# Kernel tuning notes

Measured on AMD Instinct MI355X. Metric: run time of the kernel, lower is better.

Reference implementation:

```python
import jax, jax.numpy as jnp
import numpy as np

F = 32          # fmap_size = (256 // 16) * 2
WIN = F // 8 - 1  # window = 3
HID = 160
HID4 = 640
N = 4096
Q = 16


def setup_inputs() -> dict:
    key = jax.random.key(0)
    ks = jax.random.split(key, 24)

    def lin(k, i, o):
        return jax.random.normal(k, (i, o), jnp.float32) * (1.0 / np.sqrt(i))

    return {
        "feature_pos": jax.random.normal(ks[0], (N, Q, HID), jnp.float32),
        "query_embedding": jax.random.normal(ks[1], (N, Q, HID), jnp.float32),
        "attn_matrix": jax.random.normal(ks[2], (N, Q, F * F), jnp.float32),
        "ws1": lin(ks[3], HID, HID4), "bs1": jnp.zeros((HID4,), jnp.float32),
        "ws2": lin(ks[4], HID4, HID4), "bs2": jnp.zeros((HID4,), jnp.float32),
        "ws3": lin(ks[5], HID4, HID4), "bs3": jnp.zeros((HID4,), jnp.float32),
        "ws4": lin(ks[6], HID4, 1), "bs4": jnp.zeros((1,), jnp.float32),
        "wp1": lin(ks[7], HID, HID4), "bp1": jnp.zeros((HID4,), jnp.float32),
        "wp2": lin(ks[8], HID4, HID4), "bp2": jnp.zeros((HID4,), jnp.float32),
        "wp3": lin(ks[9], HID4, HID4), "bp3": jnp.zeros((HID4,), jnp.float32),
        "wp4": lin(ks[10], HID4, 4), "bp4": jnp.zeros((4,), jnp.float32),
    }


def _mlp(x, w1, b1, w2, b2, w3, b3, w4, b4):
    h = jax.nn.relu(x @ w1 + b1)
    h = jax.nn.relu(h @ w2 + b2)
    h = jax.nn.relu(h @ w3 + b3)
    return h @ w4 + b4


def _gauss_blur3(x):
    # torchvision GaussianBlur(3, sigma=1.0): separable 3-tap, reflect padding
    e = np.exp(-0.5)
    k = jnp.asarray([e, 1.0, e], jnp.float32) / np.float32(1.0 + 2.0 * e)
    xp = jnp.pad(x, ((0, 0), (1, 1), (0, 0)), mode="reflect")
    x = k[0] * xp[:, :-2] + k[1] * xp[:, 1:-1] + k[2] * xp[:, 2:]
    xp = jnp.pad(x, ((0, 0), (0, 0), (1, 1)), mode="reflect")
    return k[0] * xp[:, :, :-2] + k[1] * xp[:, :, 1:-1] + k[2] * xp[:, :, 2:]


def _process_attnmap(am):
    # am: [N, F, F]
    n = am.shape[0]
    ab = _gauss_blur3(am)
    ab = (ab - ab.mean(axis=(1, 2), keepdims=True)) / jnp.std(ab, axis=(1, 2), keepdims=True, ddof=1)
    idx = jnp.argmax(ab.reshape(n, -1), axis=1)
    px = (idx % F).astype(jnp.int32)
    py = (idx // F).astype(jnp.int32)
    # vectorized windowed mean of clamped sigmoid (masked instead of per-sample slicing)
    s = jnp.clip(jax.nn.sigmoid(am), 1e-4, 1.0 - 1e-4)
    pos = jnp.arange(F)
    colmask = ((pos[None, :] >= jnp.maximum(0, px - WIN)[:, None]) &
               (pos[None, :] < jnp.minimum(F, px + WIN)[:, None])).astype(s.dtype)  # [N,F]
    rowmask = ((pos[None, :] >= jnp.maximum(0, py - WIN)[:, None]) &
               (pos[None, :] < jnp.minimum(F, py + WIN)[:, None])).astype(s.dtype)
    colsum = s.sum(axis=1)  # [N,F] sum over rows -> per-column totals
    rowsum = s.sum(axis=2)  # [N,F] sum over cols -> per-row totals
    tempx = (colsum * colmask).sum(axis=1) / (F * colmask.sum(axis=1))
    tempy = (rowsum * rowmask).sum(axis=1) / (F * rowmask.sum(axis=1))
    prepos = jnp.stack([px, py], axis=1).astype(jnp.float32)          # [N,2]
    presize = jnp.stack([tempx, tempy], axis=1) * np.float32(F)        # [N,2]
    return prepos, presize


def reference(feature_pos, query_embedding, attn_matrix,
              ws1, bs1, ws2, bs2, ws3, bs3, ws4, bs4,
              wp1, bp1, wp2, bp2, wp3, bp3, wp4, bp4):
    n = query_embedding.shape[0]
    qe = query_embedding.mean(axis=1)   # [N, HID]
    fp = feature_pos.mean(axis=1)       # [N, HID]
    am = attn_matrix.mean(axis=1).reshape(n, F, F)
    score = _mlp(qe, ws1, bs1, ws2, bs2, ws3, bs3, ws4, bs4).reshape(n)
    bbox_info = _mlp(fp, wp1, bp1, wp2, bp2, wp3, bp3, wp4, bp4)  # [N,4]
    sizeoffset = jnp.clip(bbox_info[:, :2], -2.0, 2.0)
    posoffset = jnp.clip(bbox_info[:, 2:], -2.0, 2.0)
    prepos, presize = _process_attnmap(am)
    xy = (prepos + posoffset) / np.float32(F)
    wh = (presize + sizeoffset) / np.float32(F)
    xy = xy - 0.5 * wh  # predict_center
    bbox = jnp.concatenate([xy, wh], axis=1)
    return bbox, score
```

## Files before the change

### kernel.cpp

```cpp
#include <hip/hip_runtime.h>
#include <hip/hip_bf16.h>
#include <stdint.h>

#define HID 160
#define HID4 640
#define FDIM 32
#define NPIX 1024

#define GK0 0.27406862f
#define GK1 0.45186276f

typedef __attribute__((ext_vector_type(8))) short short8;
typedef __attribute__((ext_vector_type(4))) float f32x4;

__device__ __forceinline__ ushort f2b(float f) {
  union { float f; uint32_t u; } v; v.f = f;
  uint32_t u = v.u;
  u += 0x7fffu + ((u >> 16) & 1u);
  return (ushort)(u >> 16);
}
__device__ __forceinline__ float b2f(ushort s) {
  union { uint32_t u; float f; } v; v.u = ((uint32_t)s) << 16;
  return v.f;
}

__global__ __launch_bounds__(256) void attn_kernel(const float* __restrict__ attn,
                                                   float* __restrict__ pp) {
  const int n = blockIdx.x;
  const int tid = threadIdx.x;
  __shared__ float am[FDIM][FDIM + 1];
  __shared__ float tmp[FDIM][FDIM + 1];
  __shared__ float bl[FDIM][FDIM + 1];
  __shared__ float rowsum[FDIM], colsum[FDIM];
  __shared__ float redv[4];
  __shared__ int redi[4];

  const float* base = attn + (size_t)n * (16 * NPIX);
  float4 a = make_float4(0.f, 0.f, 0.f, 0.f);
#pragma unroll
  for (int q = 0; q < 16; ++q) {
    float4 v = *(const float4*)(base + q * NPIX + tid * 4);
    a.x += v.x; a.y += v.y; a.z += v.z; a.w += v.w;
  }
  {
    const int f0 = tid * 4;
    const int r = f0 >> 5, c = f0 & 31;
    am[r][c + 0] = a.x * 0.0625f;
    am[r][c + 1] = a.y * 0.0625f;
    am[r][c + 2] = a.z * 0.0625f;
    am[r][c + 3] = a.w * 0.0625f;
  }
  __syncthreads();
  for (int f = tid; f < NPIX; f += 256) {
    int r = f >> 5, c = f & 31;
    int rm = (r == 0) ? 1 : r - 1;
    int rp = (r == 31) ? 30 : r + 1;
    tmp[r][c] = GK0 * am[rm][c] + GK1 * am[r][c] + GK0 * am[rp][c];
  }
  __syncthreads();
  for (int f = tid; f < NPIX; f += 256) {
    int r = f >> 5, c = f & 31;
    int cm = (c == 0) ? 1 : c - 1;
    int cp = (c == 31) ? 30 : c + 1;
    bl[r][c] = GK0 * tmp[r][cm] + GK1 * tmp[r][c] + GK0 * tmp[r][cp];
  }
  __syncthreads();
  float bv = -1e30f; int bi = 0;
  for (int f = tid; f < NPIX; f += 256) {
    float v = bl[f >> 5][f & 31];
    if (v > bv || (v == bv && f < bi)) { bv = v; bi = f; }
  }
  for (int off = 32; off > 0; off >>= 1) {
    float ov = __shfl_down(bv, off);
    int oi = __shfl_down(bi, off);
    if (ov > bv || (ov == bv && oi < bi)) { bv = ov; bi = oi; }
  }
  if ((tid & 63) == 0) { redv[tid >> 6] = bv; redi[tid >> 6] = bi; }
  for (int f = tid; f < NPIX; f += 256) {
    int r = f >> 5, c = f & 31;
    float s = 1.f / (1.f + expf(-am[r][c]));
    tmp[r][c] = fminf(fmaxf(s, 1e-4f), 0.9999f);
  }
  __syncthreads();
  if (tid < 32) {
    float s = 0.f;
    for (int c = 0; c < 32; ++c) s += tmp[tid][c];
    rowsum[tid] = s;
  } else if (tid < 64) {
    int c = tid - 32;
    float s = 0.f;
    for (int r = 0; r < 32; ++r) s += tmp[r][c];
    colsum[c] = s;
  }
  __syncthreads();
  if (tid == 0) {
    float bestv = redv[0]; int besti = redi[0];
    for (int w = 1; w < 4; ++w)
      if (redv[w] > bestv || (redv[w] == bestv && redi[w] < besti)) {
        bestv = redv[w]; besti = redi[w];
      }
    int px = besti & 31, py = besti >> 5;
    int c0 = max(0, px - 3), c1 = min(32, px + 3);
    float sx = 0.f;
    for (int c = c0; c < c1; ++c) sx += colsum[c];
    float psx = (sx / (32.f * (float)(c1 - c0))) * 32.f;
    int r0 = max(0, py - 3), r1 = min(32, py + 3);
    float sy = 0.f;
    for (int r = r0; r < r1; ++r) sy += rowsum[r];
    float psy = (sy / (32.f * (float)(r1 - r0))) * 32.f;
    pp[n * 4 + 0] = (float)px;
    pp[n * 4 + 1] = (float)py;
    pp[n * 4 + 2] = psx;
    pp[n * 4 + 3] = psy;
  }
}

__global__ __launch_bounds__(256) void mean_kernel(const float* __restrict__ qemb,
                                                   const float* __restrict__ fpos,
                                                   ushort* __restrict__ qe_b,
                                                   ushort* __restrict__ fp_b,
                                                   int total) {
  int idx = blockIdx.x * 256 + threadIdx.x;
  if (idx >= 2 * total) return;
  const float* src; ushort* dst; int i;
  if (idx < total) { src = qemb; dst = qe_b; i = idx; }
  else             { src = fpos; dst = fp_b; i = idx - total; }
  int nn = i / HID, h = i - nn * HID;
  const float* p = src + (size_t)nn * (16 * HID) + h;
  float s = 0.f;
#pragma unroll
  for (int q = 0; q < 16; ++q) s += p[q * HID];
  dst[i] = f2b(s * 0.0625f);
}

__global__ __launch_bounds__(256) void transpose_cast(const float* __restrict__ in,
                                                      ushort* __restrict__ out, int K) {
  __shared__ float t[32][33];
  const int bx = blockIdx.x * 32;
  const int by = blockIdx.y * 32;
  const int lx = threadIdx.x;
  const int ly = threadIdx.y;
#pragma unroll
  for (int i = 0; i < 4; ++i)
    t[ly + i * 8][lx] = in[(size_t)(by + ly + i * 8) * HID4 + bx + lx];
  __syncthreads();
#pragma unroll
  for (int i = 0; i < 4; ++i)
    out[(size_t)(bx + ly + i * 8) * K + by + lx] = f2b(t[lx][ly + i * 8]);
}

template <int K>
__global__ __launch_bounds__(256) void gemm_relu(
    const ushort* __restrict__ A0, const ushort* __restrict__ A1,
    const ushort* __restrict__ W0, const ushort* __restrict__ W1,
    const float* __restrict__ B0, const float* __restrict__ B1,
    ushort* __restrict__ O0, ushort* __restrict__ O1) {
  const int chain = blockIdx.z;
  const ushort* A = chain ? A1 : A0;
  const ushort* W = chain ? W1 : W0;
  const float* bias = chain ? B1 : B0;
  ushort* O = chain ? O1 : O0;

  __shared__ ushort la[64][40];
  __shared__ ushort lb[64][40];

  const int tid = threadIdx.x;
  const int bm = blockIdx.y * 64;
  const int bn = blockIdx.x * 64;
  const int lane = tid & 63;
  const int wid = tid >> 6;
  const int wr = (wid >> 1) * 32;
  const int wc = (wid & 1) * 32;
  const int srow = tid >> 2;
  const int sseg = (tid & 3) * 8;
  const int l15 = lane & 15;
  const int kq = (lane >> 4) * 8;

  f32x4 acc[2][2] = {};
  for (int k0 = 0; k0 < K; k0 += 32) {
    uint4 av = *(const uint4*)(A + (size_t)(bm + srow) * K + k0 + sseg);
    uint4 wv = *(const uint4*)(W + (size_t)(bn + srow) * K + k0 + sseg);
    __syncthreads();
    *(uint4*)(&la[srow][sseg]) = av;
    *(uint4*)(&lb[srow][sseg]) = wv;
    __syncthreads();
    short8 af0 = *(const short8*)(&la[wr + l15][kq]);
    short8 af1 = *(const short8*)(&la[wr + 16 + l15][kq]);
    short8 bf0 = *(const short8*)(&lb[wc + l15][kq]);
    short8 bf1 = *(const short8*)(&lb[wc + 16 + l15][kq]);
    acc[0][0] = __builtin_amdgcn_mfma_f32_16x16x32_bf16(af0, bf0, acc[0][0], 0, 0, 0);
    acc[0][1] = __builtin_amdgcn_mfma_f32_16x16x32_bf16(af0, bf1, acc[0][1], 0, 0, 0);
    acc[1][0] = __builtin_amdgcn_mfma_f32_16x16x32_bf16(af1, bf0, acc[1][0], 0, 0, 0);
    acc[1][1] = __builtin_amdgcn_mfma_f32_16x16x32_bf16(af1, bf1, acc[1][1], 0, 0, 0);
  }
#pragma unroll
  for (int mi = 0; mi < 2; ++mi)
#pragma unroll
    for (int nj = 0; nj < 2; ++nj) {
      const int col = bn + wc + nj * 16 + l15;
      const float bcol = bias[col];
#pragma unroll
      for (int b = 0; b < 4; ++b) {
        const int row = bm + wr + mi * 16 + (lane >> 4) * 4 + b;
        float v = acc[mi][nj][b] + bcol;
        v = fmaxf(v, 0.f);
        O[(size_t)row * HID4 + col] = f2b(v);
      }
    }
}

__global__ __launch_bounds__(256) void final_kernel(
    const ushort* __restrict__ hs, const ushort* __restrict__ hp,
    const float* __restrict__ ws4, const float* __restrict__ bs4,
    const float* __restrict__ wp4, const float* __restrict__ bp4,
    const float* __restrict__ pp, float* __restrict__ out, int N) {
  const int wid = threadIdx.x >> 6;
  const int lane = threadIdx.x & 63;
  const int n = blockIdx.x * 4 + wid;
  if (n >= N) return;
  const ushort* hsr = hs + (size_t)n * HID4;
  const ushort* hpr = hp + (size_t)n * HID4;
  float sc = 0.f, b0 = 0.f, b1 = 0.f, b2 = 0.f, b3 = 0.f;
  for (int j = lane; j < HID4; j += 64) {
    float h1 = b2f(hsr[j]);
    sc += h1 * ws4[j];
    float h2 = b2f(hpr[j]);
    b0 += h2 * wp4[j * 4 + 0];
    b1 += h2 * wp4[j * 4 + 1];
    b2 += h2 * wp4[j * 4 + 2];
    b3 += h2 * wp4[j * 4 + 3];
  }
  for (int off = 32; off > 0; off >>= 1) {
    sc += __shfl_down(sc, off);
    b0 += __shfl_down(b0, off);
    b1 += __shfl_down(b1, off);
    b2 += __shfl_down(b2, off);
    b3 += __shfl_down(b3, off);
  }
  if (lane == 0) {
    sc += bs4[0];
    b0 += bp4[0]; b1 += bp4[1]; b2 += bp4[2]; b3 += bp4[3];
    float so0 = fminf(fmaxf(b0, -2.f), 2.f);
    float so1 = fminf(fmaxf(b1, -2.f), 2.f);
    float po0 = fminf(fmaxf(b2, -2.f), 2.f);
    float po1 = fminf(fmaxf(b3, -2.f), 2.f);
    float px = pp[n * 4 + 0], py = pp[n * 4 + 1];
    float psx = pp[n * 4 + 2], psy = pp[n * 4 + 3];
    float wh0 = (psx + so0) * (1.f / 32.f);
    float wh1 = (psy + so1) * (1.f / 32.f);
    float xy0 = (px + po0) * (1.f / 32.f) - 0.5f * wh0;
    float xy1 = (py + po1) * (1.f / 32.f) - 0.5f * wh1;
    out[n * 4 + 0] = xy0;
    out[n * 4 + 1] = xy1;
    out[n * 4 + 2] = wh0;
    out[n * 4 + 3] = wh1;
    out[(size_t)4 * N + n] = sc;
  }
}

extern "C" void kernel_launch(void* const* d_in, const int* in_sizes, int n_in,
                              void* d_out, int out_size, void* d_ws, size_t ws_size,
                              hipStream_t stream) {
  const float* fpos = (const float*)d_in[0];
  const float* qemb = (const float*)d_in[1];
  const float* attn = (const float*)d_in[2];
  const float* ws1 = (const float*)d_in[3];
  const float* bs1 = (const float*)d_in[4];
  const float* ws2 = (const float*)d_in[5];
  const float* bs2 = (const float*)d_in[6];
  const float* ws3 = (const float*)d_in[7];
  const float* bs3 = (const float*)d_in[8];
  const float* ws4 = (const float*)d_in[9];
  const float* bs4 = (const float*)d_in[10];
  const float* wp1 = (const float*)d_in[11];
  const float* bp1 = (const float*)d_in[12];
  const float* wp2 = (const float*)d_in[13];
  const float* bp2 = (const float*)d_in[14];
  const float* wp3 = (const float*)d_in[15];
  const float* bp3 = (const float*)d_in[16];
  const float* wp4 = (const float*)d_in[17];
  const float* bp4 = (const float*)d_in[18];
  float* out = (float*)d_out;

  const int N = in_sizes[0] / (16 * HID);

  char* ws = (char*)d_ws;
  const size_t SZ_QE = (size_t)N * HID * 2;
  const size_t SZ_W1 = (size_t)HID4 * HID * 2;
  const size_t SZ_W2 = (size_t)HID4 * HID4 * 2;
  const size_t SZ_H  = (size_t)N * HID4 * 2;
  size_t off = 0;
  ushort* qe_b = (ushort*)(ws + off); off += SZ_QE;
  ushort* fp_b = (ushort*)(ws + off); off += SZ_QE;
  ushort* wts1 = (ushort*)(ws + off); off += SZ_W1;
  ushort* wtp1 = (ushort*)(ws + off); off += SZ_W1;
  ushort* wts2 = (ushort*)(ws + off); off += SZ_W2;
  ushort* wtp2 = (ushort*)(ws + off); off += SZ_W2;
  ushort* wts3 = (ushort*)(ws + off); off += SZ_W2;
  ushort* wtp3 = (ushort*)(ws + off); off += SZ_W2;
  ushort* hsA  = (ushort*)(ws + off); off += SZ_H;
  ushort* hsB  = (ushort*)(ws + off); off += SZ_H;
  ushort* hpA  = (ushort*)(ws + off); off += SZ_H;
  ushort* hpB  = (ushort*)(ws + off); off += SZ_H;
  float*  pp   = (float*)(ws + off);  off += (size_t)N * 4 * 4;

  attn_kernel<<<N, 256, 0, stream>>>(attn, pp);

  const int total = N * HID;
  mean_kernel<<<(2 * total + 255) / 256, 256, 0, stream>>>(qemb, fpos, qe_b, fp_b, total);

  dim3 tb(32, 8);
  transpose_cast<<<dim3(HID4 / 32, HID / 32), tb, 0, stream>>>(ws1, wts1, HID);
  transpose_cast<<<dim3(HID4 / 32, HID / 32), tb, 0, stream>>>(wp1, wtp1, HID);
  transpose_cast<<<dim3(HID4 / 32, HID4 / 32), tb, 0, stream>>>(ws2, wts2, HID4);
  transpose_cast<<<dim3(HID4 / 32, HID4 / 32), tb, 0, stream>>>(wp2, wtp2, HID4);
  transpose_cast<<<dim3(HID4 / 32, HID4 / 32), tb, 0, stream>>>(ws3, wts3, HID4);
  transpose_cast<<<dim3(HID4 / 32, HID4 / 32), tb, 0, stream>>>(wp3, wtp3, HID4);

  dim3 gg(HID4 / 64, N / 64, 2);
  gemm_relu<HID><<<gg, 256, 0, stream>>>(qe_b, fp_b, wts1, wtp1, bs1, bp1, hsA, hpA);
  gemm_relu<HID4><<<gg, 256, 0, stream>>>(hsA, hpA, wts2, wtp2, bs2, bp2, hsB, hpB);
  gemm_relu<HID4><<<gg, 256, 0, stream>>>(hsB, hpB, wts3, wtp3, bs3, bp3, hsA, hpA);

  final_kernel<<<(N + 3) / 4, 256, 0, stream>>>(hsA, hpA, ws4, bs4, wp4, bp4, pp, out, N);
}
```

Measured before the change: 144.9 us.

## Fuse attn processing into GEMM launches, enlarge GEMM tiles, merge prep kernels

Spreads the per-sample attention-map processing blocks across the three GEMM launches, so the memory-bound attn reduction runs alongside the compute-bound GEMMs. GEMM tiles grow from 64x64 to 128x128 with a 4x4 MFMA accumulator per wave, and operands are staged with global_load_lds direct-to-LDS loads. The mean and six transpose-cast launches merge into one prep kernel, and the mean uses float2 loads. This cuts launch count and improves data reuse, but raises register pressure and LDS use. It also leaves only 320 GEMM blocks per launch, and with no double buffering each k-step waits on its loads.

```diff
diff --git a/kernel.cpp b/kernel.cpp
--- a/kernel.cpp
+++ b/kernel.cpp
@@ -24,17 +24,30 @@
   return v.f;
 }
 
-__global__ __launch_bounds__(256) void attn_kernel(const float* __restrict__ attn,
-                                                   float* __restrict__ pp) {
-  const int n = blockIdx.x;
+__device__ __forceinline__ void gload16(const ushort* g, ushort* l) {
+  __builtin_amdgcn_global_load_lds(
+      (const __attribute__((address_space(1))) void*)g,
+      (__attribute__((address_space(3))) void*)l, 16, 0, 0);
+}
+
+union SMem {
+  struct {
+    ushort la[128 * 32];
+    ushort lb[128 * 32];
+  } g;
+  struct {
+    float am[FDIM][FDIM + 1];
+    float tmp[FDIM][FDIM + 1];
+    float bl[FDIM][FDIM + 1];
+    float rowsum[FDIM], colsum[FDIM];
+    float redv[4];
+    int redi[4];
+  } a;
+};
+
+__device__ void attn_block(SMem& sm, const float* __restrict__ attn,
+                           float* __restrict__ pp, int n) {
   const int tid = threadIdx.x;
-  __shared__ float am[FDIM][FDIM + 1];
-  __shared__ float tmp[FDIM][FDIM + 1];
-  __shared__ float bl[FDIM][FDIM + 1];
-  __shared__ float rowsum[FDIM], colsum[FDIM];
-  __shared__ float redv[4];
-  __shared__ int redi[4];
-
   const float* base = attn + (size_t)n * (16 * NPIX);
   float4 a = make_float4(0.f, 0.f, 0.f, 0.f);
 #pragma unroll
@@ -45,29 +58,29 @@
   {
     const int f0 = tid * 4;
     const int r = f0 >> 5, c = f0 & 31;
-    am[r][c + 0] = a.x * 0.0625f;
-    am[r][c + 1] = a.y * 0.0625f;
-    am[r][c + 2] = a.z * 0.0625f;
-    am[r][c + 3] = a.w * 0.0625f;
+    sm.a.am[r][c + 0] = a.x * 0.0625f;
+    sm.a.am[r][c + 1] = a.y * 0.0625f;
+    sm.a.am[r][c + 2] = a.z * 0.0625f;
+    sm.a.am[r][c + 3] = a.w * 0.0625f;
   }
   __syncthreads();
   for (int f = tid; f < NPIX; f += 256) {
     int r = f >> 5, c = f & 31;
     int rm = (r == 0) ? 1 : r - 1;
     int rp = (r == 31) ? 30 : r + 1;
-    tmp[r][c] = GK0 * am[rm][c] + GK1 * am[r][c] + GK0 * am[rp][c];
+    sm.a.tmp[r][c] = GK0 * sm.a.am[rm][c] + GK1 * sm.a.am[r][c] + GK0 * sm.a.am[rp][c];
   }
   __syncthreads();
   for (int f = tid; f < NPIX; f += 256) {
     int r = f >> 5, c = f & 31;
     int cm = (c == 0) ? 1 : c - 1;
     int cp = (c == 31) ? 30 : c + 1;
-    bl[r][c] = GK0 * tmp[r][cm] + GK1 * tmp[r][c] + GK0 * tmp[r][cp];
+    sm.a.bl[r][c] = GK0 * sm.a.tmp[r][cm] + GK1 * sm.a.tmp[r][c] + GK0 * sm.a.tmp[r][cp];
   }
   __syncthreads();
   float bv = -1e30f; int bi = 0;
   for (int f = tid; f < NPIX; f += 256) {
-    float v = bl[f >> 5][f & 31];
+    float v = sm.a.bl[f >> 5][f & 31];
     if (v > bv || (v == bv && f < bi)) { bv = v; bi = f; }
   }
   for (int off = 32; off > 0; off >>= 1) {
@@ -75,38 +88,38 @@
     int oi = __shfl_down(bi, off);
     if (ov > bv || (ov == bv && oi < bi)) { bv = ov; bi = oi; }
   }
-  if ((tid & 63) == 0) { redv[tid >> 6] = bv; redi[tid >> 6] = bi; }
+  if ((tid & 63) == 0) { sm.a.redv[tid >> 6] = bv; sm.a.redi[tid >> 6] = bi; }
   for (int f = tid; f < NPIX; f += 256) {
     int r = f >> 5, c = f & 31;
-    float s = 1.f / (1.f + expf(-am[r][c]));
-    tmp[r][c] = fminf(fmaxf(s, 1e-4f), 0.9999f);
+    float s = 1.f / (1.f + expf(-sm.a.am[r][c]));
+    sm.a.tmp[r][c] = fminf(fmaxf(s, 1e-4f), 0.9999f);
   }
   __syncthreads();
   if (tid < 32) {
     float s = 0.f;
-    for (int c = 0; c < 32; ++c) s += tmp[tid][c];
-    rowsum[tid] = s;
+    for (int c = 0; c < 32; ++c) s += sm.a.tmp[tid][c];
+    sm.a.rowsum[tid] = s;
   } else if (tid < 64) {
     int c = tid - 32;
     float s = 0.f;
-    for (int r = 0; r < 32; ++r) s += tmp[r][c];
-    colsum[c] = s;
+    for (int r = 0; r < 32; ++r) s += sm.a.tmp[r][c];
+    sm.a.colsum[c] = s;
   }
   __syncthreads();
   if (tid == 0) {
-    float bestv = redv[0]; int besti = redi[0];
+    float bestv = sm.a.redv[0]; int besti = sm.a.redi[0];
     for (int w = 1; w < 4; ++w)
-      if (redv[w] > bestv || (redv[w] == bestv && redi[w] < besti)) {
-        bestv = redv[w]; besti = redi[w];
+      if (sm.a.redv[w] > bestv || (sm.a.redv[w] == bestv && sm.a.redi[w] < besti)) {
+        bestv = sm.a.redv[w]; besti = sm.a.redi[w];
       }
     int px = besti & 31, py = besti >> 5;
     int c0 = max(0, px - 3), c1 = min(32, px + 3);
     float sx = 0.f;
-    for (int c = c0; c < c1; ++c) sx += colsum[c];
+    for (int c = c0; c < c1; ++c) sx += sm.a.colsum[c];
     float psx = (sx / (32.f * (float)(c1 - c0))) * 32.f;
     int r0 = max(0, py - 3), r1 = min(32, py + 3);
     float sy = 0.f;
-    for (int r = r0; r < r1; ++r) sy += rowsum[r];
+    for (int r = r0; r < r1; ++r) sy += sm.a.rowsum[r];
     float psy = (sy / (32.f * (float)(r1 - r0))) * 32.f;
     pp[n * 4 + 0] = (float)px;
     pp[n * 4 + 1] = (float)py;
@@ -115,98 +128,141 @@
   }
 }
 
-__global__ __launch_bounds__(256) void mean_kernel(const float* __restrict__ qemb,
-                                                   const float* __restrict__ fpos,
-                                                   ushort* __restrict__ qe_b,
-                                                   ushort* __restrict__ fp_b,
-                                                   int total) {
-  int idx = blockIdx.x * 256 + threadIdx.x;
-  if (idx >= 2 * total) return;
-  const float* src; ushort* dst; int i;
-  if (idx < total) { src = qemb; dst = qe_b; i = idx; }
-  else             { src = fpos; dst = fp_b; i = idx - total; }
-  int nn = i / HID, h = i - nn * HID;
-  const float* p = src + (size_t)nn * (16 * HID) + h;
-  float s = 0.f;
-#pragma unroll
-  for (int q = 0; q < 16; ++q) s += p[q * HID];
-  dst[i] = f2b(s * 0.0625f);
-}
-
-__global__ __launch_bounds__(256) void transpose_cast(const float* __restrict__ in,
-                                                      ushort* __restrict__ out, int K) {
-  __shared__ float t[32][33];
-  const int bx = blockIdx.x * 32;
-  const int by = blockIdx.y * 32;
-  const int lx = threadIdx.x;
-  const int ly = threadIdx.y;
-#pragma unroll
-  for (int i = 0; i < 4; ++i)
-    t[ly + i * 8][lx] = in[(size_t)(by + ly + i * 8) * HID4 + bx + lx];
-  __syncthreads();
-#pragma unroll
-  for (int i = 0; i < 4; ++i)
-    out[(size_t)(bx + ly + i * 8) * K + by + lx] = f2b(t[lx][ly + i * 8]);
-}
-
 template <int K>
-__global__ __launch_bounds__(256) void gemm_relu(
+__global__ __launch_bounds__(256) void gemm_attn(
     const ushort* __restrict__ A0, const ushort* __restrict__ A1,
     const ushort* __restrict__ W0, const ushort* __restrict__ W1,
     const float* __restrict__ B0, const float* __restrict__ B1,
-    ushort* __restrict__ O0, ushort* __restrict__ O1) {
-  const int chain = blockIdx.z;
+    ushort* __restrict__ O0, ushort* __restrict__ O1,
+    const float* __restrict__ attn, float* __restrict__ pp,
+    int attn_base, int n_gemm) {
+  __shared__ SMem sm;
+  const int tid = threadIdx.x;
+
+  if ((int)blockIdx.x >= n_gemm) {
+    attn_block(sm, attn, pp, attn_base + (int)blockIdx.x - n_gemm);
+    return;
+  }
+
+  const int bid = blockIdx.x;
+  const int half = n_gemm >> 1;
+  const int chain = bid >= half;
+  const int r = chain ? bid - half : bid;
+  const int bn = (r % 5) * 128;
+  const int bm = (r / 5) * 128;
   const ushort* A = chain ? A1 : A0;
   const ushort* W = chain ? W1 : W0;
   const float* bias = chain ? B1 : B0;
   ushort* O = chain ? O1 : O0;
 
-  __shared__ ushort la[64][40];
-  __shared__ ushort lb[64][40];
-
-  const int tid = threadIdx.x;
-  const int bm = blockIdx.y * 64;
-  const int bn = blockIdx.x * 64;
   const int lane = tid & 63;
   const int wid = tid >> 6;
-  const int wr = (wid >> 1) * 32;
-  const int wc = (wid & 1) * 32;
-  const int srow = tid >> 2;
-  const int sseg = (tid & 3) * 8;
+  const int wr = (wid >> 1) * 64;
+  const int wc = (wid & 1) * 64;
   const int l15 = lane & 15;
   const int kq = (lane >> 4) * 8;
 
-  f32x4 acc[2][2] = {};
+  const int rstage = tid >> 2;
+  const int cstage = (tid & 3) * 8;
+  ushort* la = sm.g.la;
+  ushort* lb = sm.g.lb;
+  const int ldsbase = wid * 512;
+
+  f32x4 acc[4][4] = {};
   for (int k0 = 0; k0 < K; k0 += 32) {
-    uint4 av = *(const uint4*)(A + (size_t)(bm + srow) * K + k0 + sseg);
-    uint4 wv = *(const uint4*)(W + (size_t)(bn + srow) * K + k0 + sseg);
+#pragma unroll
+    for (int j = 0; j < 2; ++j) {
+      gload16(A + (size_t)(bm + j * 64 + rstage) * K + k0 + cstage,
+              la + j * 2048 + ldsbase);
+      gload16(W + (size_t)(bn + j * 64 + rstage) * K + k0 + cstage,
+              lb + j * 2048 + ldsbase);
+    }
     __syncthreads();
-    *(uint4*)(&la[srow][sseg]) = av;
-    *(uint4*)(&lb[srow][sseg]) = wv;
+    short8 af[4], bf[4];
+#pragma unroll
+    for (int i = 0; i < 4; ++i) {
+      af[i] = *(const short8*)(la + (wr + i * 16 + l15) * 32 + kq);
+      bf[i] = *(const short8*)(lb + (wc + i * 16 + l15) * 32 + kq);
+    }
+#pragma unroll
+    for (int mi = 0; mi < 4; ++mi)
+#pragma unroll
+      for (int nj = 0; nj < 4; ++nj)
+        acc[mi][nj] = __builtin_amdgcn_mfma_f32_16x16x32_bf16(af[mi], bf[nj], acc[mi][nj], 0, 0, 0);
     __syncthreads();
-    short8 af0 = *(const short8*)(&la[wr + l15][kq]);
-    short8 af1 = *(const short8*)(&la[wr + 16 + l15][kq]);
-    short8 bf0 = *(const short8*)(&lb[wc + l15][kq]);
-    short8 bf1 = *(const short8*)(&lb[wc + 16 + l15][kq]);
-    acc[0][0] = __builtin_amdgcn_mfma_f32_16x16x32_bf16(af0, bf0, acc[0][0], 0, 0, 0);
-    acc[0][1] = __builtin_amdgcn_mfma_f32_16x16x32_bf16(af0, bf1, acc[0][1], 0, 0, 0);
-    acc[1][0] = __builtin_amdgcn_mfma_f32_16x16x32_bf16(af1, bf0, acc[1][0], 0, 0, 0);
-    acc[1][1] = __builtin_amdgcn_mfma_f32_16x16x32_bf16(af1, bf1, acc[1][1], 0, 0, 0);
-  }
-#pragma unroll
-  for (int mi = 0; mi < 2; ++mi)
-#pragma unroll
-    for (int nj = 0; nj < 2; ++nj) {
-      const int col = bn + wc + nj * 16 + l15;
-      const float bcol = bias[col];
+  }
+
+#pragma unroll
+  for (int nj = 0; nj < 4; ++nj) {
+    const int col = bn + wc + nj * 16 + l15;
+    const float bcol = bias[col];
+#pragma unroll
+    for (int mi = 0; mi < 4; ++mi) {
+      const int rbase = bm + wr + mi * 16 + (lane >> 4) * 4;
 #pragma unroll
       for (int b = 0; b < 4; ++b) {
-        const int row = bm + wr + mi * 16 + (lane >> 4) * 4 + b;
         float v = acc[mi][nj][b] + bcol;
-        v = fmaxf(v, 0.f);
-        O[(size_t)row * HID4 + col] = f2b(v);
+        O[(size_t)(rbase + b) * HID4 + col] = f2b(fmaxf(v, 0.f));
       }
     }
+  }
+}
+
+__global__ __launch_bounds__(256) void prep_kernel(
+    const float* __restrict__ qemb, const float* __restrict__ fpos,
+    ushort* __restrict__ qe_b, ushort* __restrict__ fp_b,
+    const float* __restrict__ ws1, ushort* __restrict__ wts1,
+    const float* __restrict__ wp1, ushort* __restrict__ wtp1,
+    const float* __restrict__ ws2, ushort* __restrict__ wts2,
+    const float* __restrict__ wp2, ushort* __restrict__ wtp2,
+    const float* __restrict__ ws3, ushort* __restrict__ wts3,
+    const float* __restrict__ wp3, ushort* __restrict__ wtp3,
+    int n_mean_blocks, int total) {
+  const int tid = threadIdx.x;
+  const int bid = blockIdx.x;
+
+  if (bid < n_mean_blocks) {
+    int idx = bid * 256 + tid;
+    const int pairs = total >> 1;
+    const float* src; ushort* dst; int i;
+    if (idx < pairs) { src = qemb; dst = qe_b; i = idx; }
+    else             { src = fpos; dst = fp_b; i = idx - pairs; }
+    int nn = i / (HID / 2);
+    int h = (i - nn * (HID / 2)) * 2;
+    const float* p = src + (size_t)nn * (16 * HID) + h;
+    float sx = 0.f, sy = 0.f;
+#pragma unroll
+    for (int q = 0; q < 16; ++q) {
+      float2 v = *(const float2*)(p + q * HID);
+      sx += v.x; sy += v.y;
+    }
+    ushort2 o;
+    o.x = f2b(sx * 0.0625f);
+    o.y = f2b(sy * 0.0625f);
+    *(ushort2*)(dst + (size_t)nn * HID + h) = o;
+    return;
+  }
+
+  int r = bid - n_mean_blocks;
+  const float* in; ushort* out; int K;
+  if (r < 100)       { in = ws1; out = wts1; K = HID; }
+  else if (r < 200)  { in = wp1; out = wtp1; K = HID; r -= 100; }
+  else if (r < 600)  { in = ws2; out = wts2; K = HID4; r -= 200; }
+  else if (r < 1000) { in = wp2; out = wtp2; K = HID4; r -= 600; }
+  else if (r < 1400) { in = ws3; out = wts3; K = HID4; r -= 1000; }
+  else               { in = wp3; out = wtp3; K = HID4; r -= 1400; }
+  const int bx = (r % 20) * 32;
+  const int by = (r / 20) * 32;
+  const int lx = tid & 31;
+  const int ly = tid >> 5;
+  __shared__ float t[32][33];
+#pragma unroll
+  for (int i = 0; i < 4; ++i)
+    t[ly + i * 8][lx] = in[(size_t)(by + ly + i * 8) * HID4 + bx + lx];
+  __syncthreads();
+#pragma unroll
+  for (int i = 0; i < 4; ++i)
+    out[(size_t)(bx + ly + i * 8) * K + by + lx] = f2b(t[lx][ly + i * 8]);
 }
 
 __global__ __launch_bounds__(256) void final_kernel(
@@ -304,23 +360,23 @@
   ushort* hpB  = (ushort*)(ws + off); off += SZ_H;
   float*  pp   = (float*)(ws + off);  off += (size_t)N * 4 * 4;
 
-  attn_kernel<<<N, 256, 0, stream>>>(attn, pp);
-
   const int total = N * HID;
-  mean_kernel<<<(2 * total + 255) / 256, 256, 0, stream>>>(qemb, fpos, qe_b, fp_b, total);
-
-  dim3 tb(32, 8);
-  transpose_cast<<<dim3(HID4 / 32, HID / 32), tb, 0, stream>>>(ws1, wts1, HID);
-  transpose_cast<<<dim3(HID4 / 32, HID / 32), tb, 0, stream>>>(wp1, wtp1, HID);
-  transpose_cast<<<dim3(HID4 / 32, HID4 / 32), tb, 0, stream>>>(ws2, wts2, HID4);
-  transpose_cast<<<dim3(HID4 / 32, HID4 / 32), tb, 0, stream>>>(wp2, wtp2, HID4);
-  transpose_cast<<<dim3(HID4 / 32, HID4 / 32), tb, 0, stream>>>(ws3, wts3, HID4);
-  transpose_cast<<<dim3(HID4 / 32, HID4 / 32), tb, 0, stream>>>(wp3, wtp3, HID4);
-
-  dim3 gg(HID4 / 64, N / 64, 2);
-  gemm_relu<HID><<<gg, 256, 0, stream>>>(qe_b, fp_b, wts1, wtp1, bs1, bp1, hsA, hpA);
-  gemm_relu<HID4><<<gg, 256, 0, stream>>>(hsA, hpA, wts2, wtp2, bs2, bp2, hsB, hpB);
-  gemm_relu<HID4><<<gg, 256, 0, stream>>>(hsB, hpB, wts3, wtp3, bs3, bp3, hsA, hpA);
+  const int n_mean_blocks = (2 * (total >> 1) + 255) / 256;
+  prep_kernel<<<n_mean_blocks + 1800, 256, 0, stream>>>(
+      qemb, fpos, qe_b, fp_b, ws1, wts1, wp1, wtp1, ws2, wts2, wp2, wtp2,
+      ws3, wts3, wp3, wtp3, n_mean_blocks, total);
+
+  const int n_gemm = 2 * 5 * (N / 128);
+  const int a2 = (N * 29) / 100;
+  const int a3 = a2;
+  const int a1 = N - a2 - a3;
+
+  gemm_attn<HID><<<n_gemm + a1, 256, 0, stream>>>(
+      qe_b, fp_b, wts1, wtp1, bs1, bp1, hsA, hpA, attn, pp, 0, n_gemm);
+  gemm_attn<HID4><<<n_gemm + a2, 256, 0, stream>>>(
+      hsA, hpA, wts2, wtp2, bs2, bp2, hsB, hpB, attn, pp, a1, n_gemm);
+  gemm_attn<HID4><<<n_gemm + a3, 256, 0, stream>>>(
+      hsB, hpB, wts3, wtp3, bs3, bp3, hsA, hpA, attn, pp, a1 + a2, n_gemm);
 
   final_kernel<<<(N + 3) / 4, 256, 0, stream>>>(hsA, hpA, ws4, bs4, wp4, bp4, pp, out, N);
 }
```

After: 119.4 us. 17.6% less time.
